# Kernel optimization log

Hardware: AMD Instinct MI355X
Metric: run time of the kernel (lower is better)

## Reference

```python
import jax, jax.numpy as jnp
import numpy as np

B, DM, H, D, N = 1024, 512, 8, 64, 81  # batch, d_model, nhead, depth, tokens (9x9)


def setup_inputs() -> dict:
    key = jax.random.key(0)
    k1, k2, k3, k4, k5 = jax.random.split(key, 5)
    return {
        "x": jax.random.normal(k1, (B, DM, 9, 9), dtype=jnp.float32),
        "qkv_w": jax.random.normal(k2, (3 * DM, DM), dtype=jnp.float32) * 0.02,
        "qkv_b": jax.random.normal(k3, (3 * DM,), dtype=jnp.float32) * 0.02,
        "rel_h": jax.random.normal(k4, (1, H, D, 1, 9), dtype=jnp.float32),
        "rel_w": jax.random.normal(k5, (1, H, D, 9, 1), dtype=jnp.float32),
    }


def reference(x, qkv_w, qkv_b, rel_h, rel_w):
    b = x.shape[0]
    xf = x.reshape(b, DM, N)                                   # [B, C, 81]
    # 1x1 conv == channel matmul
    qkv = jnp.einsum('oc,bcn->bon', qkv_w, xf) + qkv_b[None, :, None]
    q, k, v = jnp.split(qkv, 3, axis=1)                         # each [B, DM, 81]
    q = q.reshape(b, H, D, N).transpose(0, 1, 3, 2)             # [B, H, 81, D]
    k = k.reshape(b, H, D, N)                                   # [B, H, D, 81]
    v = v.reshape(b, H, D, N).transpose(0, 1, 3, 2)             # [B, H, 81, D]
    content_content = jnp.einsum('bhnd,bhdm->bhnm', q, k)       # [B, H, 81, 81]
    r = (rel_h + rel_w).reshape(H, D, N)                        # broadcast add -> [H, D, 81]
    content_position = jnp.einsum('bhnd,hdm->bhnm', q, r)       # [B, H, 81, 81]
    attention = jax.nn.softmax(content_content + content_position, axis=-1)
    out = jnp.einsum('bhnm,bhmd->bhnd', attention, v)            # [B, H, 81, D]
    return out.transpose(0, 1, 3, 2).reshape(b, DM, 9, 9)
```

## Files before the change

### kernel.cpp

```cpp
#include <hip/hip_runtime.h>
#include <hip/hip_bf16.h>
#include <cstdint>
#include <cstddef>

#define NB 1024
#define DM 512
#define NH 8
#define HD 64
#define NT 81
#define O3 1536
#define NP 96

typedef __bf16 bf16x8 __attribute__((ext_vector_type(8)));
typedef float  f32x4  __attribute__((ext_vector_type(4)));
typedef unsigned short us8 __attribute__((ext_vector_type(8)));

__device__ __forceinline__ unsigned short f2bf(float f) {
    unsigned u = __builtin_bit_cast(unsigned, f);
    u += 0x7fffu + ((u >> 16) & 1u);
    return (unsigned short)(u >> 16);
}
__device__ __forceinline__ float bf2f(unsigned short h) {
    unsigned u = ((unsigned)h) << 16;
    return __builtin_bit_cast(float, u);
}
__device__ __forceinline__ bf16x8 ld8(const unsigned short* p) {
    return __builtin_bit_cast(bf16x8, *(const us8*)p);
}
__device__ __forceinline__ void async16(void* lds, const void* g) {
    __builtin_amdgcn_global_load_lds(
        (const __attribute__((address_space(1))) void*)g,
        (__attribute__((address_space(3))) void*)lds, 16, 0, 0);
}

__global__ void conv_w(const float* __restrict__ w, unsigned short* __restrict__ wb, int n) {
    int i = blockIdx.x * 256 + threadIdx.x;
    if (i < n) wb[i] = f2bf(w[i]);
}

__global__ __launch_bounds__(256) void transpose_x(
    const float* __restrict__ x, unsigned short* __restrict__ xT)
{
    __shared__ float sT[64][85];
    const int tid = threadIdx.x;
    const int b  = blockIdx.x >> 3;
    const int c0 = (blockIdx.x & 7) * 64;
    const float* xb = x + ((size_t)b * DM + c0) * NT;

    const int nn = tid & 31, cc0 = tid >> 5;
    for (int i = 0; i < 8; ++i) {
        int cc = cc0 + i * 8;
        const float* xr = xb + (size_t)cc * NT;
        #pragma unroll
        for (int j = 0; j < 3; ++j) {
            int n = nn + 32 * j;
            if (n < NT) sT[cc][n] = xr[n];
        }
    }
    __syncthreads();

    const int ci = tid & 7, n0 = tid >> 3;
    for (int i = 0; i < 3; ++i) {
        int n = n0 + 32 * i;
        us8 v;
        #pragma unroll
        for (int j = 0; j < 8; ++j) {
            float f = (n < NT) ? sT[ci * 8 + j][n] : 0.f;
            v[j] = f2bf(f);
        }
        *(us8*)(xT + ((size_t)b * NP + n) * DM + c0 + ci * 8) = v;
    }
}

#define OT 256
#define KC 32

__global__ __launch_bounds__(256, 3) void qkv_gemm_a(
    const unsigned short* __restrict__ xT,
    const unsigned short* __restrict__ wb,
    const float* __restrict__ bias,
    const float* __restrict__ relh,
    const float* __restrict__ relw,
    unsigned short* __restrict__ qkv)
{
    __shared__ __align__(16) unsigned short sW[2][OT * KC];
    __shared__ __align__(16) unsigned short sX[2][NP * KC];

    const int tid  = threadIdx.x;
    const int lane = tid & 63;
    const int wv   = tid >> 6;
    const int D    = blockIdx.x;
    const int s    = D >> 3;
    const int b    = (D & 7) * (NB / 8) + s / 6;
    const int ot   = s % 6;
    const int o0   = ot * OT;
    const int r16  = lane & 15;
    const int q8   = (lane >> 4) * 8;
    const int sq8  = q8 ^ ((r16 & 3) * 8);

    f32x4 acc[4][6];
    #pragma unroll
    for (int i = 0; i < 4; ++i)
        #pragma unroll
        for (int j = 0; j < 6; ++j)
            acc[i][j] = (f32x4){0.f, 0.f, 0.f, 0.f};

    const unsigned short* xb = xT + (size_t)b * NP * DM;

    auto stage = [&](int bi, int kc) {
        unsigned short* dW = &sW[bi][0];
        unsigned short* dX = &sX[bi][0];
        #pragma unroll
        for (int i = 0; i < 4; ++i) {
            int ch  = i * 256 + wv * 64 + lane;
            int row = ch >> 2, cb = ch & 3;
            int cbs = cb ^ (row & 3);
            async16(dW + (i * 256 + wv * 64) * 8,
                    wb + (size_t)(o0 + row) * DM + kc + cbs * 8);
        }
        {
            int ch  = wv * 64 + lane;
            int row = ch >> 2, cb = ch & 3;
            int cbs = cb ^ (row & 3);
            async16(dX + (wv * 64) * 8, xb + (size_t)row * DM + kc + cbs * 8);
            if (wv < 2) {
                int ch2  = 256 + wv * 64 + lane;
                int row2 = ch2 >> 2, cb2 = ch2 & 3;
                int cbs2 = cb2 ^ (row2 & 3);
                async16(dX + (256 + wv * 64) * 8, xb + (size_t)row2 * DM + kc + cbs2 * 8);
            }
        }
    };

    auto compute = [&](const unsigned short* bW, const unsigned short* bX) {
        bf16x8 af[4], bfr[6];
        #pragma unroll
        for (int i = 0; i < 4; ++i)
            af[i] = ld8(&bW[(wv * 64 + i * 16 + r16) * KC + sq8]);
        #pragma unroll
        for (int nt = 0; nt < 6; ++nt)
            bfr[nt] = ld8(&bX[(nt * 16 + r16) * KC + sq8]);
        #pragma unroll
        for (int i = 0; i < 4; ++i)
            #pragma unroll
            for (int nt = 0; nt < 6; ++nt)
                acc[i][nt] = __builtin_amdgcn_mfma_f32_16x16x32_bf16(af[i], bfr[nt], acc[i][nt], 0, 0, 0);
    };

    stage(0, 0);
    __syncthreads();
    for (int ks = 0; ks < 16; ks += 2) {
        stage(1, (ks + 1) * KC);
        compute(&sW[0][0], &sX[0][0]);
        __syncthreads();
        if (ks + 2 < 16) stage(0, (ks + 2) * KC);
        compute(&sW[1][0], &sX[1][0]);
        __syncthreads();
    }

    unsigned short* qb = qkv + (size_t)b * O3 * NT;
    #pragma unroll
    for (int i = 0; i < 4; ++i) {
        int obase = o0 + (wv * 4 + i) * 16 + (lane >> 4) * 4;
        #pragma unroll
        for (int nt = 0; nt < 6; ++nt) {
            int n = nt * 16 + r16;
            if (n < NT) {
                #pragma unroll
                for (int r = 0; r < 4; ++r) {
                    int o = obase + r;
                    float v = acc[i][nt][r] + bias[o];
                    if (o >= DM && o < 2 * DM) {
                        int oo = o - DM;
                        v += relh[oo * 9 + (n % 9)] + relw[oo * 9 + (n / 9)];
                    }
                    qb[(size_t)o * NT + n] = f2bf(v);
                }
            }
        }
    }
}

#define OTILE 128
#define SWS 40
#define SXS 40

__global__ __launch_bounds__(256) void qkv_gemm_fb(
    const float* __restrict__ x,
    const unsigned short* __restrict__ wb,
    const float* __restrict__ bias,
    const float* __restrict__ relh,
    const float* __restrict__ relw,
    unsigned short* __restrict__ qkv)
{
    __shared__ unsigned short sW[OTILE * SWS];
    __shared__ unsigned short sXT[NP * SXS];

    const int tid  = threadIdx.x;
    const int lane = tid & 63;
    const int wv   = tid >> 6;
    const int b    = blockIdx.x / (O3 / OTILE);
    const int ot   = blockIdx.x % (O3 / OTILE);
    const int o0   = ot * OTILE;
    const int r16 = lane & 15;
    const int q8  = (lane >> 4) * 8;

    f32x4 acc[2][6];
    for (int i = 0; i < 2; ++i)
        for (int j = 0; j < 6; ++j)
            acc[i][j] = (f32x4){0.f, 0.f, 0.f, 0.f};

    const float* xb = x + (size_t)b * DM * NT;
    const int wr  = tid >> 2;
    const int wc  = (tid & 3) * 8;
    const int xc  = tid >> 3;
    const int xn0 = tid & 7;

    for (int kc = 0; kc < DM; kc += 32) {
        {
            us8 v0 = *(const us8*)(wb + (size_t)(o0 + wr) * DM + kc + wc);
            us8 v1 = *(const us8*)(wb + (size_t)(o0 + wr + 64) * DM + kc + wc);
            *(us8*)(&sW[wr * SWS + wc]) = v0;
            *(us8*)(&sW[(wr + 64) * SWS + wc]) = v1;
        }
        {
            const float* xr = xb + (size_t)(kc + xc) * NT;
            #pragma unroll
            for (int j = 0; j < 12; ++j) {
                int n = xn0 + 8 * j;
                float v = (n < NT) ? xr[n] : 0.f;
                sXT[n * SXS + xc] = f2bf(v);
            }
        }
        __syncthreads();
        bf16x8 af0 = ld8(&sW[((wv * 2 + 0) * 16 + r16) * SWS + q8]);
        bf16x8 af1 = ld8(&sW[((wv * 2 + 1) * 16 + r16) * SWS + q8]);
        #pragma unroll
        for (int nt = 0; nt < 6; ++nt) {
            bf16x8 bfr = ld8(&sXT[(nt * 16 + r16) * SXS + q8]);
            acc[0][nt] = __builtin_amdgcn_mfma_f32_16x16x32_bf16(af0, bfr, acc[0][nt], 0, 0, 0);
            acc[1][nt] = __builtin_amdgcn_mfma_f32_16x16x32_bf16(af1, bfr, acc[1][nt], 0, 0, 0);
        }
        __syncthreads();
    }

    unsigned short* qb = qkv + (size_t)b * O3 * NT;
    #pragma unroll
    for (int i = 0; i < 2; ++i) {
        int obase = o0 + (wv * 2 + i) * 16 + (lane >> 4) * 4;
        #pragma unroll
        for (int nt = 0; nt < 6; ++nt) {
            int n = nt * 16 + r16;
            if (n < NT) {
                #pragma unroll
                for (int r = 0; r < 4; ++r) {
                    int o = obase + r;
                    float v = acc[i][nt][r] + bias[o];
                    if (o >= DM && o < 2 * DM) {
                        int oo = o - DM;
                        v += relh[oo * 9 + (n % 9)] + relw[oo * 9 + (n / 9)];
                    }
                    qb[(size_t)o * NT + n] = f2bf(v);
                }
            }
        }
    }
}

#define SQS 72
#define SPS 104
#define SVS 104

__global__ __launch_bounds__(384, 6) void attn(
    const unsigned short* __restrict__ qkv,
    float* __restrict__ out)
{
    __shared__ __align__(16) unsigned short smem[20480];
    unsigned short* sQ   = smem;
    unsigned short* sK   = smem + 96 * SQS;
    unsigned short* sP   = smem;
    float*          sRcp = (float*)(smem + 96 * SPS);
    unsigned short* sV   = smem + 2 * 96 * SQS;

    const int tid  = threadIdx.x;
    const int lane = tid & 63;
    const int wv   = tid >> 6;
    const int c    = lane & 15;
    const int q    = lane >> 4;
    const int q8   = q * 8;
    const int b    = blockIdx.x >> 3;
    const int h    = blockIdx.x & 7;

    const unsigned short* qp = qkv + (size_t)b * O3 * NT + (size_t)(h * HD) * NT;
    const unsigned short* kp = qp + (size_t)DM * NT;
    const unsigned short* vp = qp + (size_t)(2 * DM) * NT;

    {
        const int n   = tid % 96;
        const int d2b = tid / 96;
        #pragma unroll
        for (int i = 0; i < 8; ++i) {
            int d2 = d2b * 8 + i;
            unsigned q0 = 0, q1 = 0, k0 = 0, k1 = 0;
            if (n < NT) {
                q0 = qp[(2 * d2) * NT + n]; q1 = qp[(2 * d2 + 1) * NT + n];
                k0 = kp[(2 * d2) * NT + n]; k1 = kp[(2 * d2 + 1) * NT + n];
            }
            ((unsigned*)sQ)[n * 36 + d2] = q0 | (q1 << 16);
            ((unsigned*)sK)[n * 36 + d2] = k0 | (k1 << 16);
        }
    }
    for (int idx = tid; idx < HD * 52; idx += 384) {
        int d = idx / 52, m2 = idx - d * 52;
        int m0 = 2 * m2;
        unsigned e0 = (m0 < NT)     ? (unsigned)vp[d * NT + m0]     : 0u;
        unsigned e1 = (m0 + 1 < NT) ? (unsigned)vp[d * NT + m0 + 1] : 0u;
        ((unsigned*)sV)[d * 52 + m2] = e0 | (e1 << 16);
    }
    __syncthreads();

    f32x4 acc[6];
    #pragma unroll
    for (int mt = 0; mt < 6; ++mt) acc[mt] = (f32x4){0.f, 0.f, 0.f, 0.f};
    #pragma unroll
    for (int kk = 0; kk < 2; ++kk) {
        bf16x8 qa = ld8(&sQ[(wv * 16 + c) * SQS + kk * 32 + q8]);
        #pragma unroll
        for (int mt = 0; mt < 6; ++mt) {
            bf16x8 kb = ld8(&sK[(mt * 16 + c) * SQS + kk * 32 + q8]);
            acc[mt] = __builtin_amdgcn_mfma_f32_16x16x32_bf16(qa, kb, acc[mt], 0, 0, 0);
        }
    }
    #pragma unroll
    for (int r = 0; r < 4; ++r)
        acc[5][r] = (c == 0) ? acc[5][r] : -3.0e38f;

    float rcp[4];
    #pragma unroll
    for (int r = 0; r < 4; ++r) {
        float mx = fmaxf(fmaxf(fmaxf(acc[0][r], acc[1][r]), fmaxf(acc[2][r], acc[3][r])),
                         fmaxf(acc[4][r], acc[5][r]));
        mx = fmaxf(mx, __shfl_xor(mx, 1));
        mx = fmaxf(mx, __shfl_xor(mx, 2));
        mx = fmaxf(mx, __shfl_xor(mx, 4));
        mx = fmaxf(mx, __shfl_xor(mx, 8));
        float s = 0.f;
        #pragma unroll
        for (int mt = 0; mt < 6; ++mt) {
            float e = exp2f((acc[mt][r] - mx) * 1.44269504088896f);
            acc[mt][r] = e;
            s += bf2f(f2bf(e));
        }
        s += __shfl_xor(s, 1);
        s += __shfl_xor(s, 2);
        s += __shfl_xor(s, 4);
        s += __shfl_xor(s, 8);
        rcp[r] = 1.0f / s;
    }

    __syncthreads();

    #pragma unroll
    for (int mt = 0; mt < 6; ++mt)
        #pragma unroll
        for (int r = 0; r < 4; ++r)
            sP[(wv * 16 + 4 * q + r) * SPS + mt * 16 + c] = f2bf(acc[mt][r]);
    if (c == 0) {
        #pragma unroll
        for (int r = 0; r < 4; ++r)
            sRcp[wv * 16 + 4 * q + r] = rcp[r];
    }

    f32x4 oacc[4];
    #pragma unroll
    for (int dt = 0; dt < 4; ++dt) oacc[dt] = (f32x4){0.f, 0.f, 0.f, 0.f};
    #pragma unroll
    for (int kt = 0; kt < 3; ++kt) {
        bf16x8 pb = ld8(&sP[(wv * 16 + c) * SPS + kt * 32 + q8]);
        #pragma unroll
        for (int dt = 0; dt < 4; ++dt) {
            bf16x8 va = ld8(&sV[(dt * 16 + c) * SVS + kt * 32 + q8]);
            oacc[dt] = __builtin_amdgcn_mfma_f32_16x16x32_bf16(va, pb, oacc[dt], 0, 0, 0);
        }
    }

    float* ob = out + (size_t)b * DM * NT + (size_t)(h * HD) * NT;
    const int n = wv * 16 + c;
    if (n < NT) {
        float rs = sRcp[n];
        #pragma unroll
        for (int dt = 0; dt < 4; ++dt) {
            #pragma unroll
            for (int r = 0; r < 4; ++r)
                ob[(size_t)(dt * 16 + 4 * q + r) * NT + n] = oacc[dt][r] * rs;
        }
    }
}

extern "C" void kernel_launch(void* const* d_in, const int* in_sizes, int n_in,
                              void* d_out, int out_size, void* d_ws, size_t ws_size,
                              hipStream_t stream) {
    const float* x     = (const float*)d_in[0];
    const float* qkv_w = (const float*)d_in[1];
    const float* qkv_b = (const float*)d_in[2];
    const float* rel_h = (const float*)d_in[3];
    const float* rel_w = (const float*)d_in[4];
    float* out = (float*)d_out;

    unsigned short* qkv = (unsigned short*)d_ws;
    unsigned short* wb  = qkv + (size_t)NB * O3 * NT;
    unsigned short* xT  = wb + (size_t)O3 * DM;
    size_t need = ((size_t)NB * O3 * NT + (size_t)O3 * DM + (size_t)NB * NP * DM) * 2;

    conv_w<<<dim3((O3 * DM + 255) / 256), dim3(256), 0, stream>>>(qkv_w, wb, O3 * DM);
    if (ws_size >= need) {
        transpose_x<<<dim3(NB * 8), dim3(256), 0, stream>>>(x, xT);
        qkv_gemm_a<<<dim3(NB * 6), dim3(256), 0, stream>>>(xT, wb, qkv_b, rel_h, rel_w, qkv);
    } else {
        qkv_gemm_fb<<<dim3(NB * 12), dim3(256), 0, stream>>>(x, wb, qkv_b, rel_h, rel_w, qkv);
    }
    attn<<<dim3(NB * NH), dim3(384), 0, stream>>>(qkv, out);
}
```

Baseline: 755.0 us.

## Store Q/K token-major and V padded so attention reads MFMA fragments from global

The QKV GEMM epilogue now writes Q and K transposed (token-major, channel contiguous, 4-wide packed stores) and V in a padded channel-major layout with zeroed tail columns. The attention kernel then loads its MFMA operands straight from global memory instead of staging and transposing Q, K, V through shared memory, which removes that staging and a barrier and shrinks LDS use. The occupancy hint changes from 6 to 4 blocks. In exchange, operand loads are uncoalesced gathers from global/L2, K rows are fetched redundantly by every wave, and the V stores in the GEMM epilogue stay scalar.

```diff
diff --git a/kernel.cpp b/kernel.cpp
--- a/kernel.cpp
+++ b/kernel.cpp
@@ -11,9 +11,15 @@
 #define O3 1536
 #define NP 96
 
+#define VPAD 88
+#define VSZ  (512 * VPAD)
+#define QTSZ (81 * 512)
+#define PB   (VSZ + 2 * QTSZ)
+
 typedef __bf16 bf16x8 __attribute__((ext_vector_type(8)));
 typedef float  f32x4  __attribute__((ext_vector_type(4)));
 typedef unsigned short us8 __attribute__((ext_vector_type(8)));
+typedef unsigned short us4 __attribute__((ext_vector_type(4)));
 
 __device__ __forceinline__ unsigned short f2bf(float f) {
     unsigned u = __builtin_bit_cast(unsigned, f);
@@ -158,23 +164,48 @@
         __syncthreads();
     }
 
-    unsigned short* qb = qkv + (size_t)b * O3 * NT;
-    #pragma unroll
-    for (int i = 0; i < 4; ++i) {
-        int obase = o0 + (wv * 4 + i) * 16 + (lane >> 4) * 4;
-        #pragma unroll
-        for (int nt = 0; nt < 6; ++nt) {
-            int n = nt * 16 + r16;
-            if (n < NT) {
-                #pragma unroll
-                for (int r = 0; r < 4; ++r) {
-                    int o = obase + r;
-                    float v = acc[i][nt][r] + bias[o];
-                    if (o >= DM && o < 2 * DM) {
-                        int oo = o - DM;
-                        v += relh[oo * 9 + (n % 9)] + relw[oo * 9 + (n / 9)];
+    unsigned short* base = qkv + (size_t)b * PB;
+    const int sec = ot >> 1;
+    if (sec < 2) {
+        unsigned short* tb = base + VSZ + sec * QTSZ;
+        const int osec = o0 - sec * 512;
+        #pragma unroll
+        for (int i = 0; i < 4; ++i) {
+            int obase = osec + (wv * 4 + i) * 16 + (lane >> 4) * 4;
+            #pragma unroll
+            for (int nt = 0; nt < 6; ++nt) {
+                int n = nt * 16 + r16;
+                if (n < NT) {
+                    us4 pk;
+                    #pragma unroll
+                    for (int r = 0; r < 4; ++r) {
+                        int o = obase + r;
+                        float v = acc[i][nt][r] + bias[sec * 512 + o];
+                        if (sec == 1)
+                            v += relh[o * 9 + (n % 9)] + relw[o * 9 + (n / 9)];
+                        pk[r] = f2bf(v);
                     }
-                    qb[(size_t)o * NT + n] = f2bf(v);
+                    *(us4*)(tb + (size_t)n * 512 + obase) = pk;
+                }
+            }
+        }
+    } else {
+        unsigned short* vb = base;
+        const int osec = o0 - 1024;
+        #pragma unroll
+        for (int i = 0; i < 4; ++i) {
+            int obase = osec + (wv * 4 + i) * 16 + (lane >> 4) * 4;
+            #pragma unroll
+            for (int nt = 0; nt < 6; ++nt) {
+                int n = nt * 16 + r16;
+                if (n < VPAD) {
+                    #pragma unroll
+                    for (int r = 0; r < 4; ++r) {
+                        int o = obase + r;
+                        unsigned short sv = 0;
+                        if (n < NT) sv = f2bf(acc[i][nt][r] + bias[1024 + o]);
+                        vb[(size_t)o * VPAD + n] = sv;
+                    }
                 }
             }
         }
@@ -244,43 +275,62 @@
         __syncthreads();
     }
 
-    unsigned short* qb = qkv + (size_t)b * O3 * NT;
-    #pragma unroll
-    for (int i = 0; i < 2; ++i) {
-        int obase = o0 + (wv * 2 + i) * 16 + (lane >> 4) * 4;
-        #pragma unroll
-        for (int nt = 0; nt < 6; ++nt) {
-            int n = nt * 16 + r16;
-            if (n < NT) {
-                #pragma unroll
-                for (int r = 0; r < 4; ++r) {
-                    int o = obase + r;
-                    float v = acc[i][nt][r] + bias[o];
-                    if (o >= DM && o < 2 * DM) {
-                        int oo = o - DM;
-                        v += relh[oo * 9 + (n % 9)] + relw[oo * 9 + (n / 9)];
+    unsigned short* base = qkv + (size_t)b * PB;
+    const int sec = ot >> 2;
+    if (sec < 2) {
+        unsigned short* tb = base + VSZ + sec * QTSZ;
+        const int osec = o0 - sec * 512;
+        #pragma unroll
+        for (int i = 0; i < 2; ++i) {
+            int obase = osec + (wv * 2 + i) * 16 + (lane >> 4) * 4;
+            #pragma unroll
+            for (int nt = 0; nt < 6; ++nt) {
+                int n = nt * 16 + r16;
+                if (n < NT) {
+                    us4 pk;
+                    #pragma unroll
+                    for (int r = 0; r < 4; ++r) {
+                        int o = obase + r;
+                        float v = acc[i][nt][r] + bias[sec * 512 + o];
+                        if (sec == 1)
+                            v += relh[o * 9 + (n % 9)] + relw[o * 9 + (n / 9)];
+                        pk[r] = f2bf(v);
                     }
-                    qb[(size_t)o * NT + n] = f2bf(v);
+                    *(us4*)(tb + (size_t)n * 512 + obase) = pk;
                 }
             }
         }
-    }
-}
-
-#define SQS 72
+    } else {
+        unsigned short* vb = base;
+        const int osec = o0 - 1024;
+        #pragma unroll
+        for (int i = 0; i < 2; ++i) {
+            int obase = osec + (wv * 2 + i) * 16 + (lane >> 4) * 4;
+            #pragma unroll
+            for (int nt = 0; nt < 6; ++nt) {
+                int n = nt * 16 + r16;
+                if (n < VPAD) {
+                    #pragma unroll
+                    for (int r = 0; r < 4; ++r) {
+                        int o = obase + r;
+                        unsigned short sv = 0;
+                        if (n < NT) sv = f2bf(acc[i][nt][r] + bias[1024 + o]);
+                        vb[(size_t)o * VPAD + n] = sv;
+                    }
+                }
+            }
+        }
+    }
+}
+
 #define SPS 104
-#define SVS 104
-
-__global__ __launch_bounds__(384, 6) void attn(
+
+__global__ __launch_bounds__(384, 4) void attn(
     const unsigned short* __restrict__ qkv,
     float* __restrict__ out)
 {
-    __shared__ __align__(16) unsigned short smem[20480];
-    unsigned short* sQ   = smem;
-    unsigned short* sK   = smem + 96 * SQS;
-    unsigned short* sP   = smem;
-    float*          sRcp = (float*)(smem + 96 * SPS);
-    unsigned short* sV   = smem + 2 * 96 * SQS;
+    __shared__ __align__(16) unsigned short sP[96 * SPS];
+    __shared__ float sRcp[96];
 
     const int tid  = threadIdx.x;
     const int lane = tid & 63;
@@ -291,43 +341,22 @@
     const int b    = blockIdx.x >> 3;
     const int h    = blockIdx.x & 7;
 
-    const unsigned short* qp = qkv + (size_t)b * O3 * NT + (size_t)(h * HD) * NT;
-    const unsigned short* kp = qp + (size_t)DM * NT;
-    const unsigned short* vp = qp + (size_t)(2 * DM) * NT;
-
-    {
-        const int n   = tid % 96;
-        const int d2b = tid / 96;
-        #pragma unroll
-        for (int i = 0; i < 8; ++i) {
-            int d2 = d2b * 8 + i;
-            unsigned q0 = 0, q1 = 0, k0 = 0, k1 = 0;
-            if (n < NT) {
-                q0 = qp[(2 * d2) * NT + n]; q1 = qp[(2 * d2 + 1) * NT + n];
-                k0 = kp[(2 * d2) * NT + n]; k1 = kp[(2 * d2 + 1) * NT + n];
-            }
-            ((unsigned*)sQ)[n * 36 + d2] = q0 | (q1 << 16);
-            ((unsigned*)sK)[n * 36 + d2] = k0 | (k1 << 16);
-        }
-    }
-    for (int idx = tid; idx < HD * 52; idx += 384) {
-        int d = idx / 52, m2 = idx - d * 52;
-        int m0 = 2 * m2;
-        unsigned e0 = (m0 < NT)     ? (unsigned)vp[d * NT + m0]     : 0u;
-        unsigned e1 = (m0 + 1 < NT) ? (unsigned)vp[d * NT + m0 + 1] : 0u;
-        ((unsigned*)sV)[d * 52 + m2] = e0 | (e1 << 16);
-    }
-    __syncthreads();
-
+    const unsigned short* vg = qkv + (size_t)b * PB;
+    const unsigned short* qg = vg + VSZ;
+    const unsigned short* kg = qg + QTSZ;
+    const int hofs = h * HD;
+
+    const int nq = min(wv * 16 + c, 80);
     f32x4 acc[6];
     #pragma unroll
     for (int mt = 0; mt < 6; ++mt) acc[mt] = (f32x4){0.f, 0.f, 0.f, 0.f};
     #pragma unroll
     for (int kk = 0; kk < 2; ++kk) {
-        bf16x8 qa = ld8(&sQ[(wv * 16 + c) * SQS + kk * 32 + q8]);
+        bf16x8 qa = ld8(qg + (size_t)nq * 512 + hofs + kk * 32 + q8);
         #pragma unroll
         for (int mt = 0; mt < 6; ++mt) {
-            bf16x8 kb = ld8(&sK[(mt * 16 + c) * SQS + kk * 32 + q8]);
+            int mrow = (mt * 16 + c < NT) ? (mt * 16 + c) : 80;
+            bf16x8 kb = ld8(kg + (size_t)mrow * 512 + hofs + kk * 32 + q8);
             acc[mt] = __builtin_amdgcn_mfma_f32_16x16x32_bf16(qa, kb, acc[mt], 0, 0, 0);
         }
     }
@@ -358,8 +387,6 @@
         rcp[r] = 1.0f / s;
     }
 
-    __syncthreads();
-
     #pragma unroll
     for (int mt = 0; mt < 6; ++mt)
         #pragma unroll
@@ -379,12 +406,12 @@
         bf16x8 pb = ld8(&sP[(wv * 16 + c) * SPS + kt * 32 + q8]);
         #pragma unroll
         for (int dt = 0; dt < 4; ++dt) {
-            bf16x8 va = ld8(&sV[(dt * 16 + c) * SVS + kt * 32 + q8]);
+            bf16x8 va = ld8(vg + (size_t)(hofs + dt * 16 + c) * VPAD + kt * 32 + q8);
             oacc[dt] = __builtin_amdgcn_mfma_f32_16x16x32_bf16(va, pb, oacc[dt], 0, 0, 0);
         }
     }
 
-    float* ob = out + (size_t)b * DM * NT + (size_t)(h * HD) * NT;
+    float* ob = out + (size_t)b * DM * NT + (size_t)hofs * NT;
     const int n = wv * 16 + c;
     if (n < NT) {
         float rs = sRcp[n];
@@ -408,9 +435,9 @@
     float* out = (float*)d_out;
 
     unsigned short* qkv = (unsigned short*)d_ws;
-    unsigned short* wb  = qkv + (size_t)NB * O3 * NT;
+    unsigned short* wb  = qkv + (size_t)NB * PB;
     unsigned short* xT  = wb + (size_t)O3 * DM;
-    size_t need = ((size_t)NB * O3 * NT + (size_t)O3 * DM + (size_t)NB * NP * DM) * 2;
+    size_t need = ((size_t)NB * PB + (size_t)O3 * DM + (size_t)NB * NP * DM) * 2;
 
     conv_w<<<dim3((O3 * DM + 255) / 256), dim3(256), 0, stream>>>(qkv_w, wb, O3 * DM);
     if (ws_size >= need) {
```

Result: no change. 767.8 us (+1.7%).
